# Performance work log

Measured on AMD Instinct MI355X. Metric: run time of the kernel, lower is better.

The kernel has to match this reference:

```python
import jax, jax.numpy as jnp
import numpy as np

WS = 8          # window size
HEADS = 2
EPS = 1e-5      # torch LayerNorm default

def setup_inputs() -> dict:
    key = jax.random.key(0)
    ks = jax.random.split(key, 8)
    B, C, H, W = 4, 64, 512, 512
    hid = 128
    s = 0.02
    return {
        "x": jax.random.normal(ks[0], (B, C, H, W), jnp.float32),
        "norm1_g": jnp.ones((C,), jnp.float32),
        "norm1_b": jnp.zeros((C,), jnp.float32),
        "in_w": s * jax.random.normal(ks[1], (3 * C, C), jnp.float32),
        "in_b": jnp.zeros((3 * C,), jnp.float32),
        "out_w": s * jax.random.normal(ks[2], (C, C), jnp.float32),
        "out_b": jnp.zeros((C,), jnp.float32),
        "proj_w": s * jax.random.normal(ks[3], (C, C), jnp.float32),
        "proj_b": jnp.zeros((C,), jnp.float32),
        "norm2_g": jnp.ones((C,), jnp.float32),
        "norm2_b": jnp.zeros((C,), jnp.float32),
        "mlp_w1": s * jax.random.normal(ks[4], (hid, C), jnp.float32),
        "mlp_b1": jnp.zeros((hid,), jnp.float32),
        "mlp_w2": s * jax.random.normal(ks[5], (C, hid), jnp.float32),
        "mlp_b2": jnp.zeros((C,), jnp.float32),
    }

def _ln(t, g, b):
    m = jnp.mean(t, axis=-1, keepdims=True)
    v = jnp.mean(jnp.square(t - m), axis=-1, keepdims=True)
    return (t - m) * jax.lax.rsqrt(v + EPS) * g + b

def _block(x, norm1_g, norm1_b, in_w, in_b, out_w, out_b,
           proj_w, proj_b, norm2_g, norm2_b, mlp_w1, mlp_b1, mlp_w2, mlp_b2):
    B, C, H, W = x.shape
    ws = WS
    # H, W divisible by ws => pad_h = pad_w = 0 (module pads otherwise)
    # window partition: (B,C,H,W) -> (B*nWh*nWw, ws*ws, C)
    t = x.reshape(B, C, H // ws, ws, W // ws, ws)
    t = jnp.transpose(t, (0, 2, 4, 3, 5, 1))            # (B, nWh, nWw, ws, ws, C)
    tokens = t.reshape(-1, ws * ws, C)                  # (nw, T, C)
    nw, T, _ = tokens.shape
    dh = C // HEADS

    tn = _ln(tokens, norm1_g, norm1_b)
    # packed qkv projection (torch MultiheadAttention in_proj)
    qkv = tn @ in_w.T + in_b                            # (nw, T, 3C)
    q, k, v = jnp.split(qkv, 3, axis=-1)
    q = q.reshape(nw, T, HEADS, dh)
    k = k.reshape(nw, T, HEADS, dh)
    v = v.reshape(nw, T, HEADS, dh)
    scale = 1.0 / jnp.sqrt(jnp.asarray(dh, x.dtype))
    scores = jnp.einsum('nqhd,nkhd->nhqk', q, k) * scale  # (nw, H, T, T)
    attn = jax.nn.softmax(scores, axis=-1)
    o = jnp.einsum('nhqk,nkhd->nqhd', attn, v).reshape(nw, T, C)
    o = o @ out_w.T + out_b                             # MHA out_proj
    o = o @ proj_w.T + proj_b                           # extra proj
    tokens = tokens + o

    tn2 = _ln(tokens, norm2_g, norm2_b)
    h = jax.nn.gelu(tn2 @ mlp_w1.T + mlp_b1, approximate=False)
    tokens = tokens + (h @ mlp_w2.T + mlp_b2)

    # window reverse: (nw, T, C) -> (B, C, H, W)
    t = tokens.reshape(B, H // ws, W // ws, ws, ws, C)
    t = jnp.transpose(t, (0, 5, 1, 3, 2, 4))
    return t.reshape(B, C, H, W)

def reference(x, norm1_g, norm1_b, in_w, in_b, out_w, out_b,
              proj_w, proj_b, norm2_g, norm2_b, mlp_w1, mlp_b1, mlp_w2, mlp_b2):
    return _block(x, norm1_g, norm1_b, in_w, in_b, out_w, out_b,
                  proj_w, proj_b, norm2_g, norm2_b, mlp_w1, mlp_b1, mlp_w2, mlp_b2)
```

## Files before the change

kernel.cpp:

```cpp
#include <hip/hip_runtime.h>
#include <math.h>

#define HWs (512*512)

typedef short  s8v __attribute__((ext_vector_type(8)));
typedef short  s4v __attribute__((ext_vector_type(4)));
typedef float  f4v __attribute__((ext_vector_type(4)));

__device__ __forceinline__ float lo16(unsigned int u){ union{unsigned int i; float f;} z; z.i=u<<16;         return z.f; }
__device__ __forceinline__ float hi16(unsigned int u){ union{unsigned int i; float f;} z; z.i=u&0xffff0000u; return z.f; }
__device__ __forceinline__ unsigned int cvtpk(float lo, float hi){
  unsigned int r; asm("v_cvt_pk_bf16_f32 %0, %1, %2" : "=v"(r) : "v"(lo), "v"(hi)); return r;
}
__device__ __forceinline__ unsigned short f2bf_rne(float f){
  union{float g; unsigned int u;} a; a.g=f;
  unsigned int r = a.u + 0x7fffu + ((a.u>>16)&1u);
  return (unsigned short)(r>>16);
}
__device__ __forceinline__ void st8(void* p, unsigned int a, unsigned int b){
  union{ unsigned int u[2]; s4v v; } z; z.u[0]=a; z.u[1]=b;
  *(s4v*)p = z.v;
}
__device__ __forceinline__ void st16(void* p, unsigned int a, unsigned int b, unsigned int c, unsigned int d){
  union{ unsigned int u[4]; s8v v; } z; z.u[0]=a; z.u[1]=b; z.u[2]=c; z.u[3]=d;
  *(s8v*)p = z.v;
}

#define SWZ(row) (((((row)&7) ^ (((row)>>3)&7)))<<4)

__global__ void conv_wb(const float* __restrict__ inw, const float* __restrict__ w1,
                        const float* __restrict__ w2, unsigned short* __restrict__ ws){
  int i = blockIdx.x*256 + threadIdx.x;
  if (i < 12288)      ws[i] = f2bf_rne(inw[i]);
  else if (i < 20480) ws[i] = f2bf_rne(w1[i-12288]);
  else                ws[i] = f2bf_rne(w2[i-20480]);
}

__global__ void fuse_proj_kernel(const float* __restrict__ out_w, const float* __restrict__ out_b,
                                 const float* __restrict__ proj_w, const float* __restrict__ proj_b,
                                 unsigned short* __restrict__ wf_bf, float* __restrict__ bfv){
  int i = blockIdx.x*256 + threadIdx.x;
  if (i >= 64*64) return;
  int c = i>>6, k = i&63;
  float acc = 0.f;
  for (int m=0;m<64;m++) acc += proj_w[c*64+m]*out_w[m*64+k];
  wf_bf[i] = f2bf_rne(acc);
  if (k==0){
    float ab = proj_b[c];
    for (int m=0;m<64;m++) ab += proj_w[c*64+m]*out_b[m];
    bfv[c] = ab;
  }
}

__global__ __launch_bounds__(512,4) void hat_main(
    const float* __restrict__ x,
    const float* __restrict__ n1g, const float* __restrict__ n1b,
    const float* __restrict__ inb,
    const unsigned short* __restrict__ wbf,
    const float* __restrict__ bfv,
    const float* __restrict__ n2g, const float* __restrict__ n2b,
    const float* __restrict__ b1, const float* __restrict__ b2,
    float* __restrict__ out)
{
  __shared__ __align__(16) unsigned char lds[65536];
  #define RA 0
  #define RB 8192
  #define RC 16384
  #define RD 24576

  const int t = threadIdx.x;
  const int l = t & 63;
  const int g = (l>>4)&3, c = l&15;
  const int w  = t>>6;
  const int tm = w>>1;
  const int wb = (w&1)<<15;
  const int cb = t>>7;
  const int pr = (t>>4)&7;
  const int pc = t&15;
  const int tok = pr*8 + (pc&7);
  const int wtb = ((pc>>3)&1)<<15;

  const int n = blockIdx.x;
  const int ww2 = n&31, wh=(n>>5)&63, b=n>>11;
  const size_t pix = (size_t)(wh*8+pr)*512 + ww2*16 + pc;
  const float* xp = x + ((size_t)b*64 + 16*cb)*HWs + pix;

  const unsigned short* inw_bf = wbf;
  const unsigned short* w1_bf  = wbf + 12288;
  const unsigned short* w2_bf  = wbf + 20480;
  const unsigned short* wf_bf  = wbf + 28672;

  float xr[16];
  #pragma unroll
  for (int i=0;i<16;i++) xr[i] = xp[(size_t)i*HWs];
  {
    float s1=0.f, s2=0.f;
    #pragma unroll
    for (int i=0;i<16;i++){ s1 += xr[i]; s2 += xr[i]*xr[i]; }
    *(float2*)(lds + wtb + RD + tok*32 + cb*8) = make_float2(s1, s2);
  }
  __syncthreads();

  unsigned int xres[8];
  {
    float S=0.f, SS=0.f;
    #pragma unroll
    for (int grp=0; grp<4; grp++){
      float2 p = *(const float2*)(lds + wtb + RD + tok*32 + grp*8);
      S += p.x; SS += p.y;
    }
    float mu = S*(1.f/64.f);
    float var = SS*(1.f/64.f) - mu*mu;
    float rstd = rsqrtf(var + 1e-5f);
    float tv[16];
    #pragma unroll
    for (int i=0;i<16;i++) tv[i] = (xr[i]-mu)*rstd*n1g[16*cb+i] + n1b[16*cb+i];
    #pragma unroll
    for (int j=0;j<8;j++) xres[j] = cvtpk(xr[2*j], xr[2*j+1]);
    int sw = SWZ(tok);
    st16(lds + wtb + RA + tok*128 + ((32*cb   ) ^ sw),
         cvtpk(tv[0],tv[1]), cvtpk(tv[2],tv[3]), cvtpk(tv[4],tv[5]), cvtpk(tv[6],tv[7]));
    st16(lds + wtb + RA + tok*128 + ((32*cb+16) ^ sw),
         cvtpk(tv[8],tv[9]), cvtpk(tv[10],tv[11]), cvtpk(tv[12],tv[13]), cvtpk(tv[14],tv[15]));
  }
  __syncthreads();

  const int row_a = 16*tm + c;
  const int swa = SWZ(row_a);
  const float scale = 0.17677669529663688f;

  s8v a0 = *(const s8v*)(lds + wb + RA + row_a*128 + ((16*g   ) ^ swa));
  s8v a1 = *(const s8v*)(lds + wb + RA + row_a*128 + ((64+16*g) ^ swa));
  #pragma unroll 1
  for (int chunk=0; chunk<2; chunk++){
    f4v acc[4] = {};
    #pragma unroll
    for (int tn=0;tn<4;tn++){
      s8v wf0 = *(const s8v*)(inw_bf + (64*chunk+16*tn+c)*64 + 8*g);
      s8v wf1 = *(const s8v*)(inw_bf + (64*chunk+16*tn+c)*64 + 32 + 8*g);
      acc[tn] = __builtin_amdgcn_mfma_f32_16x16x32_bf16(wf0, a0, acc[tn], 0,0,0);
      acc[tn] = __builtin_amdgcn_mfma_f32_16x16x32_bf16(wf1, a1, acc[tn], 0,0,0);
    }
    const int reg = (chunk==0) ? RB : RC;
    #pragma unroll
    for (int tn=0;tn<4;tn++){
      float4 b4 = *(const float4*)(inb + 64*chunk + 16*tn + 4*g);
      float v0=acc[tn][0]+b4.x, v1=acc[tn][1]+b4.y, v2=acc[tn][2]+b4.z, v3=acc[tn][3]+b4.w;
      if (chunk==0){ v0*=scale; v1*=scale; v2*=scale; v3*=scale; }
      st8(lds + wb + reg + row_a*128 + ((2*(16*tn+4*g)) ^ swa), cvtpk(v0,v1), cvtpk(v2,v3));
    }
  }
  {
    f4v acc[4] = {};
    #pragma unroll
    for (int tn=0;tn<4;tn++){
      s8v wf0 = *(const s8v*)(inw_bf + (128+16*tn+c)*64 + 8*g);
      s8v wf1 = *(const s8v*)(inw_bf + (128+16*tn+c)*64 + 32 + 8*g);
      acc[tn] = __builtin_amdgcn_mfma_f32_16x16x32_bf16(a0, wf0, acc[tn], 0,0,0);
      acc[tn] = __builtin_amdgcn_mfma_f32_16x16x32_bf16(a1, wf1, acc[tn], 0,0,0);
    }
    #pragma unroll
    for (int tn=0;tn<4;tn++){
      int drow = 16*tn + c;
      float bias = inb[128 + drow];
      st8(lds + wb + RD + drow*128 + ((2*(16*tm+4*g)) ^ SWZ(drow)),
          cvtpk(acc[tn][0]+bias, acc[tn][1]+bias), cvtpk(acc[tn][2]+bias, acc[tn][3]+bias));
    }
  }
  __syncthreads();

  #pragma unroll 1
  for (int h=0; h<2; h++){
    s8v qa = *(const s8v*)(lds + wb + RB + row_a*128 + ((64*h+16*g) ^ swa));
    f4v sacc[4] = {};
    #pragma unroll
    for (int tn=0;tn<4;tn++){
      int kr = 16*tn + c;
      s8v kb = *(const s8v*)(lds + wb + RC + kr*128 + ((64*h+16*g) ^ SWZ(kr)));
      sacc[tn] = __builtin_amdgcn_mfma_f32_16x16x32_bf16(kb, qa, sacc[tn], 0,0,0);
    }
    float mt[4];
    #pragma unroll
    for (int tn=0;tn<4;tn++)
      mt[tn] = fmaxf(fmaxf(sacc[tn][0],sacc[tn][1]), fmaxf(sacc[tn][2],sacc[tn][3]));
    float m = fmaxf(fmaxf(mt[0],mt[1]), fmaxf(mt[2],mt[3]));
    m = fmaxf(m, __shfl_xor(m, 16));
    m = fmaxf(m, __shfl_xor(m, 32));
    float lsum = 0.f;
    float p[4][4];
    #pragma unroll
    for (int tn=0;tn<4;tn++)
      #pragma unroll
      for (int r=0;r<4;r++){ float e = __expf(sacc[tn][r]-m); p[tn][r]=e; lsum+=e; }
    lsum += __shfl_xor(lsum, 16);
    lsum += __shfl_xor(lsum, 32);
    float inv = 1.f/lsum;
    #pragma unroll
    for (int tn=0;tn<4;tn++)
      st8(lds + wb + RA + row_a*128 + ((2*(16*tn+4*g)) ^ swa),
          cvtpk(p[tn][0]*inv, p[tn][1]*inv), cvtpk(p[tn][2]*inv, p[tn][3]*inv));
    asm volatile("" ::: "memory");
    s8v pa0 = *(const s8v*)(lds + wb + RA + row_a*128 + ((16*g   ) ^ swa));
    s8v pa1 = *(const s8v*)(lds + wb + RA + row_a*128 + ((64+16*g) ^ swa));
    #pragma unroll
    for (int tnl=0; tnl<2; tnl++){
      int vr = 32*h + 16*tnl + c;
      int svr = SWZ(vr);
      s8v vb0 = *(const s8v*)(lds + wb + RD + vr*128 + ((16*g   ) ^ svr));
      s8v vb1 = *(const s8v*)(lds + wb + RD + vr*128 + ((64+16*g) ^ svr));
      f4v oc = {};
      oc = __builtin_amdgcn_mfma_f32_16x16x32_bf16(vb0, pa0, oc, 0,0,0);
      oc = __builtin_amdgcn_mfma_f32_16x16x32_bf16(vb1, pa1, oc, 0,0,0);
      st8(lds + wb + RB + row_a*128 + ((64*h + 32*tnl + 8*g) ^ swa),
          cvtpk(oc[0], oc[1]), cvtpk(oc[2], oc[3]));
    }
  }
  __syncthreads();

  {
    s8v oa0 = *(const s8v*)(lds + wb + RB + row_a*128 + ((16*g   ) ^ swa));
    s8v oa1 = *(const s8v*)(lds + wb + RB + row_a*128 + ((64+16*g) ^ swa));
    f4v acc[4] = {};
    #pragma unroll
    for (int tn=0;tn<4;tn++){
      s8v wf0 = *(const s8v*)(wf_bf + (16*tn+c)*64 + 8*g);
      s8v wf1 = *(const s8v*)(wf_bf + (16*tn+c)*64 + 32 + 8*g);
      acc[tn] = __builtin_amdgcn_mfma_f32_16x16x32_bf16(wf0, oa0, acc[tn], 0,0,0);
      acc[tn] = __builtin_amdgcn_mfma_f32_16x16x32_bf16(wf1, oa1, acc[tn], 0,0,0);
    }
    #pragma unroll
    for (int tn=0;tn<4;tn++){
      float4 b4 = *(const float4*)(bfv + 16*tn + 4*g);
      st8(lds + wb + RC + row_a*128 + ((2*(16*tn+4*g)) ^ swa),
          cvtpk(acc[tn][0]+b4.x, acc[tn][1]+b4.y), cvtpk(acc[tn][2]+b4.z, acc[tn][3]+b4.w));
    }
  }
  __syncthreads();

  float row2[16];
  {
    int sw = SWZ(tok);
    uint4 A0 = *(const uint4*)(lds + wtb + RC + tok*128 + ((32*cb   ) ^ sw));
    uint4 A1 = *(const uint4*)(lds + wtb + RC + tok*128 + ((32*cb+16) ^ sw));
    unsigned int pr8[8] = {A0.x,A0.y,A0.z,A0.w,A1.x,A1.y,A1.z,A1.w};
    #pragma unroll
    for (int j=0;j<8;j++){
      row2[2*j]   = lo16(pr8[j]) + lo16(xres[j]);
      row2[2*j+1] = hi16(pr8[j]) + hi16(xres[j]);
    }
    float s1=0.f, s2=0.f;
    #pragma unroll
    for (int i=0;i<16;i++){ s1 += row2[i]; s2 += row2[i]*row2[i]; }
    *(float2*)(lds + wtb + RB + tok*32 + cb*8) = make_float2(s1, s2);
  }
  __syncthreads();
  {
    float S=0.f, SS=0.f;
    #pragma unroll
    for (int grp=0; grp<4; grp++){
      float2 p = *(const float2*)(lds + wtb + RB + tok*32 + grp*8);
      S += p.x; SS += p.y;
    }
    float mu2 = S*(1.f/64.f);
    float v2 = SS*(1.f/64.f) - mu2*mu2;
    float rstd2 = rsqrtf(v2 + 1e-5f);
    float tv[16];
    #pragma unroll
    for (int i=0;i<16;i++) tv[i] = (row2[i]-mu2)*rstd2*n2g[16*cb+i] + n2b[16*cb+i];
    int sw = SWZ(tok);
    st16(lds + wtb + RA + tok*128 + ((32*cb   ) ^ sw),
         cvtpk(tv[0],tv[1]), cvtpk(tv[2],tv[3]), cvtpk(tv[4],tv[5]), cvtpk(tv[6],tv[7]));
    st16(lds + wtb + RA + tok*128 + ((32*cb+16) ^ sw),
         cvtpk(tv[8],tv[9]), cvtpk(tv[10],tv[11]), cvtpk(tv[12],tv[13]), cvtpk(tv[14],tv[15]));
  }
  __syncthreads();

  {
    s8v la0 = *(const s8v*)(lds + wb + RA + row_a*128 + ((16*g   ) ^ swa));
    s8v la1 = *(const s8v*)(lds + wb + RA + row_a*128 + ((64+16*g) ^ swa));
    #pragma unroll 1
    for (int nch=0; nch<2; nch++){
      f4v acc[4] = {};
      #pragma unroll
      for (int tn=0;tn<4;tn++){
        s8v wf0 = *(const s8v*)(w1_bf + (64*nch+16*tn+c)*64 + 8*g);
        s8v wf1 = *(const s8v*)(w1_bf + (64*nch+16*tn+c)*64 + 32 + 8*g);
        acc[tn] = __builtin_amdgcn_mfma_f32_16x16x32_bf16(wf0, la0, acc[tn], 0,0,0);
        acc[tn] = __builtin_amdgcn_mfma_f32_16x16x32_bf16(wf1, la1, acc[tn], 0,0,0);
      }
      const int reg = nch ? RD : RB;
      #pragma unroll
      for (int tn=0;tn<4;tn++){
        float4 b4 = *(const float4*)(b1 + 64*nch + 16*tn + 4*g);
        float vv[4] = {acc[tn][0]+b4.x, acc[tn][1]+b4.y, acc[tn][2]+b4.z, acc[tn][3]+b4.w};
        #pragma unroll
        for (int r=0;r<4;r++){
          float v = vv[r];
          float z = v*(1.595769122f + 0.071354816f*v*v);
          vv[r] = v/(1.f + __expf(-z));
        }
        st8(lds + wb + reg + row_a*128 + ((2*(16*tn+4*g)) ^ swa), cvtpk(vv[0],vv[1]), cvtpk(vv[2],vv[3]));
      }
    }
  }
  asm volatile("" ::: "memory");
  {
    f4v acc[4] = {};
    #pragma unroll
    for (int kk=0;kk<4;kk++){
      const int reg = (kk<2) ? RB : RD;
      s8v ha = *(const s8v*)(lds + wb + reg + row_a*128 + ((64*(kk&1)+16*g) ^ swa));
      #pragma unroll
      for (int tn=0;tn<4;tn++){
        s8v wf = *(const s8v*)(w2_bf + (16*tn+c)*128 + 32*kk + 8*g);
        acc[tn] = __builtin_amdgcn_mfma_f32_16x16x32_bf16(wf, ha, acc[tn], 0,0,0);
      }
    }
    #pragma unroll
    for (int tn=0;tn<4;tn++){
      float4 b4 = *(const float4*)(b2 + 16*tn + 4*g);
      st8(lds + wb + RA + row_a*128 + ((2*(16*tn+4*g)) ^ swa),
          cvtpk(acc[tn][0]+b4.x, acc[tn][1]+b4.y), cvtpk(acc[tn][2]+b4.z, acc[tn][3]+b4.w));
    }
  }
  __syncthreads();

  {
    int sw = SWZ(tok);
    uint4 A0 = *(const uint4*)(lds + wtb + RA + tok*128 + ((32*cb   ) ^ sw));
    uint4 A1 = *(const uint4*)(lds + wtb + RA + tok*128 + ((32*cb+16) ^ sw));
    unsigned int pr8[8] = {A0.x,A0.y,A0.z,A0.w,A1.x,A1.y,A1.z,A1.w};
    float* op = out + ((size_t)b*64 + 16*cb)*HWs + pix;
    #pragma unroll
    for (int j=0;j<8;j++){
      op[(size_t)(2*j  )*HWs] = lo16(pr8[j]) + row2[2*j];
      op[(size_t)(2*j+1)*HWs] = hi16(pr8[j]) + row2[2*j+1];
    }
  }
}

extern "C" void kernel_launch(void* const* d_in, const int* in_sizes, int n_in,
                              void* d_out, int out_size, void* d_ws, size_t ws_size,
                              hipStream_t stream) {
  const float* x    = (const float*)d_in[0];
  const float* n1g  = (const float*)d_in[1];
  const float* n1b  = (const float*)d_in[2];
  const float* inw  = (const float*)d_in[3];
  const float* inb  = (const float*)d_in[4];
  const float* outw = (const float*)d_in[5];
  const float* outb = (const float*)d_in[6];
  const float* pw   = (const float*)d_in[7];
  const float* pb   = (const float*)d_in[8];
  const float* n2g  = (const float*)d_in[9];
  const float* n2b  = (const float*)d_in[10];
  const float* w1   = (const float*)d_in[11];
  const float* b1   = (const float*)d_in[12];
  const float* w2   = (const float*)d_in[13];
  const float* b2   = (const float*)d_in[14];

  unsigned short* wsu = (unsigned short*)d_ws;
  unsigned short* wf_bf = wsu + 28672;
  float* bfv = (float*)((char*)d_ws + 65536);

  hipLaunchKernelGGL(conv_wb, dim3(112), dim3(256), 0, stream, inw, w1, w2, wsu);
  hipLaunchKernelGGL(fuse_proj_kernel, dim3(16), dim3(256), 0, stream, outw, outb, pw, pb, wf_bf, bfv);
  hipLaunchKernelGGL(hat_main, dim3(8192), dim3(512), 0, stream,
                     x, n1g, n1b, inb, wsu, bfv, n2g, n2b, b1, b2, (float*)d_out);
}
```

Measured before the change: 648.8 us.

## Process one window per 256-thread block and reduce LayerNorm stats via shuffles

Each block previously handled two 8x8 windows with 512 threads and 64KB of LDS. Now each block handles a single window with 256 threads and 32KB LDS, launching twice as many blocks. The thread mapping is changed so that the four channel-group threads for a token sit in the same wavefront. This lets both LayerNorm statistic reductions use shuffles and removes two LDS round-trips and barriers. Global loads now cover 8 contiguous pixels per row instead of 16, which may reduce coalescing width.

Result: slower. 735.0 us (+13.3%).

```diff
diff --git a/kernel.cpp b/kernel.cpp
--- a/kernel.cpp
+++ b/kernel.cpp
@@ -52,7 +52,7 @@
   }
 }
 
-__global__ __launch_bounds__(512,4) void hat_main(
+__global__ __launch_bounds__(256,5) void hat_main(
     const float* __restrict__ x,
     const float* __restrict__ n1g, const float* __restrict__ n1b,
     const float* __restrict__ inb,
@@ -62,7 +62,7 @@
     const float* __restrict__ b1, const float* __restrict__ b2,
     float* __restrict__ out)
 {
-  __shared__ __align__(16) unsigned char lds[65536];
+  __shared__ __align__(16) unsigned char lds[32768];
   #define RA 0
   #define RB 8192
   #define RC 16384
@@ -71,18 +71,15 @@
   const int t = threadIdx.x;
   const int l = t & 63;
   const int g = (l>>4)&3, c = l&15;
-  const int w  = t>>6;
-  const int tm = w>>1;
-  const int wb = (w&1)<<15;
-  const int cb = t>>7;
-  const int pr = (t>>4)&7;
-  const int pc = t&15;
-  const int tok = pr*8 + (pc&7);
-  const int wtb = ((pc>>3)&1)<<15;
+  const int tm = t>>6;
+  const int s  = t&7;
+  const int cb = (t>>3)&3;
+  const int r  = ((t>>6)<<1) | ((t>>5)&1);
+  const int tok = r*8 + s;
 
   const int n = blockIdx.x;
-  const int ww2 = n&31, wh=(n>>5)&63, b=n>>11;
-  const size_t pix = (size_t)(wh*8+pr)*512 + ww2*16 + pc;
+  const int ww = n&63, wh=(n>>6)&63, b=n>>12;
+  const size_t pix = (size_t)(wh*8+r)*512 + ww*8 + s;
   const float* xp = x + ((size_t)b*64 + 16*cb)*HWs + pix;
 
   const unsigned short* inw_bf = wbf;
@@ -93,24 +90,15 @@
   float xr[16];
   #pragma unroll
   for (int i=0;i<16;i++) xr[i] = xp[(size_t)i*HWs];
+  unsigned int xres[8];
   {
     float s1=0.f, s2=0.f;
     #pragma unroll
     for (int i=0;i<16;i++){ s1 += xr[i]; s2 += xr[i]*xr[i]; }
-    *(float2*)(lds + wtb + RD + tok*32 + cb*8) = make_float2(s1, s2);
-  }
-  __syncthreads();
-
-  unsigned int xres[8];
-  {
-    float S=0.f, SS=0.f;
-    #pragma unroll
-    for (int grp=0; grp<4; grp++){
-      float2 p = *(const float2*)(lds + wtb + RD + tok*32 + grp*8);
-      S += p.x; SS += p.y;
-    }
-    float mu = S*(1.f/64.f);
-    float var = SS*(1.f/64.f) - mu*mu;
+    s1 += __shfl_xor(s1, 8);  s2 += __shfl_xor(s2, 8);
+    s1 += __shfl_xor(s1, 16); s2 += __shfl_xor(s2, 16);
+    float mu = s1*(1.f/64.f);
+    float var = s2*(1.f/64.f) - mu*mu;
     float rstd = rsqrtf(var + 1e-5f);
     float tv[16];
     #pragma unroll
@@ -118,9 +106,9 @@
     #pragma unroll
     for (int j=0;j<8;j++) xres[j] = cvtpk(xr[2*j], xr[2*j+1]);
     int sw = SWZ(tok);
-    st16(lds + wtb + RA + tok*128 + ((32*cb   ) ^ sw),
+    st16(lds + RA + tok*128 + ((32*cb   ) ^ sw),
          cvtpk(tv[0],tv[1]), cvtpk(tv[2],tv[3]), cvtpk(tv[4],tv[5]), cvtpk(tv[6],tv[7]));
-    st16(lds + wtb + RA + tok*128 + ((32*cb+16) ^ sw),
+    st16(lds + RA + tok*128 + ((32*cb+16) ^ sw),
          cvtpk(tv[8],tv[9]), cvtpk(tv[10],tv[11]), cvtpk(tv[12],tv[13]), cvtpk(tv[14],tv[15]));
   }
   __syncthreads();
@@ -129,8 +117,8 @@
   const int swa = SWZ(row_a);
   const float scale = 0.17677669529663688f;
 
-  s8v a0 = *(const s8v*)(lds + wb + RA + row_a*128 + ((16*g   ) ^ swa));
-  s8v a1 = *(const s8v*)(lds + wb + RA + row_a*128 + ((64+16*g) ^ swa));
+  s8v a0 = *(const s8v*)(lds + RA + row_a*128 + ((16*g   ) ^ swa));
+  s8v a1 = *(const s8v*)(lds + RA + row_a*128 + ((64+16*g) ^ swa));
   #pragma unroll 1
   for (int chunk=0; chunk<2; chunk++){
     f4v acc[4] = {};
@@ -147,7 +135,7 @@
       float4 b4 = *(const float4*)(inb + 64*chunk + 16*tn + 4*g);
       float v0=acc[tn][0]+b4.x, v1=acc[tn][1]+b4.y, v2=acc[tn][2]+b4.z, v3=acc[tn][3]+b4.w;
       if (chunk==0){ v0*=scale; v1*=scale; v2*=scale; v3*=scale; }
-      st8(lds + wb + reg + row_a*128 + ((2*(16*tn+4*g)) ^ swa), cvtpk(v0,v1), cvtpk(v2,v3));
+      st8(lds + reg + row_a*128 + ((2*(16*tn+4*g)) ^ swa), cvtpk(v0,v1), cvtpk(v2,v3));
     }
   }
   {
@@ -163,7 +151,7 @@
     for (int tn=0;tn<4;tn++){
       int drow = 16*tn + c;
       float bias = inb[128 + drow];
-      st8(lds + wb + RD + drow*128 + ((2*(16*tm+4*g)) ^ SWZ(drow)),
+      st8(lds + RD + drow*128 + ((2*(16*tm+4*g)) ^ SWZ(drow)),
           cvtpk(acc[tn][0]+bias, acc[tn][1]+bias), cvtpk(acc[tn][2]+bias, acc[tn][3]+bias));
     }
   }
@@ -171,12 +159,12 @@
 
   #pragma unroll 1
   for (int h=0; h<2; h++){
-    s8v qa = *(const s8v*)(lds + wb + RB + row_a*128 + ((64*h+16*g) ^ swa));
+    s8v qa = *(const s8v*)(lds + RB + row_a*128 + ((64*h+16*g) ^ swa));
     f4v sacc[4] = {};
     #pragma unroll
     for (int tn=0;tn<4;tn++){
       int kr = 16*tn + c;
-      s8v kb = *(const s8v*)(lds + wb + RC + kr*128 + ((64*h+16*g) ^ SWZ(kr)));
+      s8v kb = *(const s8v*)(lds + RC + kr*128 + ((64*h+16*g) ^ SWZ(kr)));
       sacc[tn] = __builtin_amdgcn_mfma_f32_16x16x32_bf16(kb, qa, sacc[tn], 0,0,0);
     }
     float mt[4];
@@ -191,35 +179,35 @@
     #pragma unroll
     for (int tn=0;tn<4;tn++)
       #pragma unroll
-      for (int r=0;r<4;r++){ float e = __expf(sacc[tn][r]-m); p[tn][r]=e; lsum+=e; }
+      for (int rr=0;rr<4;rr++){ float e = __expf(sacc[tn][rr]-m); p[tn][rr]=e; lsum+=e; }
     lsum += __shfl_xor(lsum, 16);
     lsum += __shfl_xor(lsum, 32);
     float inv = 1.f/lsum;
     #pragma unroll
     for (int tn=0;tn<4;tn++)
-      st8(lds + wb + RA + row_a*128 + ((2*(16*tn+4*g)) ^ swa),
+      st8(lds + RA + row_a*128 + ((2*(16*tn+4*g)) ^ swa),
           cvtpk(p[tn][0]*inv, p[tn][1]*inv), cvtpk(p[tn][2]*inv, p[tn][3]*inv));
     asm volatile("" ::: "memory");
-    s8v pa0 = *(const s8v*)(lds + wb + RA + row_a*128 + ((16*g   ) ^ swa));
-    s8v pa1 = *(const s8v*)(lds + wb + RA + row_a*128 + ((64+16*g) ^ swa));
+    s8v pa0 = *(const s8v*)(lds + RA + row_a*128 + ((16*g   ) ^ swa));
+    s8v pa1 = *(const s8v*)(lds + RA + row_a*128 + ((64+16*g) ^ swa));
     #pragma unroll
     for (int tnl=0; tnl<2; tnl++){
       int vr = 32*h + 16*tnl + c;
       int svr = SWZ(vr);
-      s8v vb0 = *(const s8v*)(lds + wb + RD + vr*128 + ((16*g   ) ^ svr));
-      s8v vb1 = *(const s8v*)(lds + wb + RD + vr*128 + ((64+16*g) ^ svr));
+      s8v vb0 = *(const s8v*)(lds + RD + vr*128 + ((16*g   ) ^ svr));
+      s8v vb1 = *(const s8v*)(lds + RD + vr*128 + ((64+16*g) ^ svr));
       f4v oc = {};
       oc = __builtin_amdgcn_mfma_f32_16x16x32_bf16(vb0, pa0, oc, 0,0,0);
       oc = __builtin_amdgcn_mfma_f32_16x16x32_bf16(vb1, pa1, oc, 0,0,0);
-      st8(lds + wb + RB + row_a*128 + ((64*h + 32*tnl + 8*g) ^ swa),
+      st8(lds + RB + row_a*128 + ((64*h + 32*tnl + 8*g) ^ swa),
           cvtpk(oc[0], oc[1]), cvtpk(oc[2], oc[3]));
     }
   }
   __syncthreads();
 
   {
-    s8v oa0 = *(const s8v*)(lds + wb + RB + row_a*128 + ((16*g   ) ^ swa));
-    s8v oa1 = *(const s8v*)(lds + wb + RB + row_a*128 + ((64+16*g) ^ swa));
+    s8v oa0 = *(const s8v*)(lds + RB + row_a*128 + ((16*g   ) ^ swa));
+    s8v oa1 = *(const s8v*)(lds + RB + row_a*128 + ((64+16*g) ^ swa));
     f4v acc[4] = {};
     #pragma unroll
     for (int tn=0;tn<4;tn++){
@@ -231,7 +219,7 @@
     #pragma unroll
     for (int tn=0;tn<4;tn++){
       float4 b4 = *(const float4*)(bfv + 16*tn + 4*g);
-      st8(lds + wb + RC + row_a*128 + ((2*(16*tn+4*g)) ^ swa),
+      st8(lds + RC + row_a*128 + ((2*(16*tn+4*g)) ^ swa),
           cvtpk(acc[tn][0]+b4.x, acc[tn][1]+b4.y), cvtpk(acc[tn][2]+b4.z, acc[tn][3]+b4.w));
     }
   }
@@ -240,8 +228,8 @@
   float row2[16];
   {
     int sw = SWZ(tok);
-    uint4 A0 = *(const uint4*)(lds + wtb + RC + tok*128 + ((32*cb   ) ^ sw));
-    uint4 A1 = *(const uint4*)(lds + wtb + RC + tok*128 + ((32*cb+16) ^ sw));
+    uint4 A0 = *(const uint4*)(lds + RC + tok*128 + ((32*cb   ) ^ sw));
+    uint4 A1 = *(const uint4*)(lds + RC + tok*128 + ((32*cb+16) ^ sw));
     unsigned int pr8[8] = {A0.x,A0.y,A0.z,A0.w,A1.x,A1.y,A1.z,A1.w};
     #pragma unroll
     for (int j=0;j<8;j++){
@@ -251,33 +239,24 @@
     float s1=0.f, s2=0.f;
     #pragma unroll
     for (int i=0;i<16;i++){ s1 += row2[i]; s2 += row2[i]*row2[i]; }
-    *(float2*)(lds + wtb + RB + tok*32 + cb*8) = make_float2(s1, s2);
-  }
-  __syncthreads();
-  {
-    float S=0.f, SS=0.f;
-    #pragma unroll
-    for (int grp=0; grp<4; grp++){
-      float2 p = *(const float2*)(lds + wtb + RB + tok*32 + grp*8);
-      S += p.x; SS += p.y;
-    }
-    float mu2 = S*(1.f/64.f);
-    float v2 = SS*(1.f/64.f) - mu2*mu2;
+    s1 += __shfl_xor(s1, 8);  s2 += __shfl_xor(s2, 8);
+    s1 += __shfl_xor(s1, 16); s2 += __shfl_xor(s2, 16);
+    float mu2 = s1*(1.f/64.f);
+    float v2 = s2*(1.f/64.f) - mu2*mu2;
     float rstd2 = rsqrtf(v2 + 1e-5f);
     float tv[16];
     #pragma unroll
     for (int i=0;i<16;i++) tv[i] = (row2[i]-mu2)*rstd2*n2g[16*cb+i] + n2b[16*cb+i];
-    int sw = SWZ(tok);
-    st16(lds + wtb + RA + tok*128 + ((32*cb   ) ^ sw),
+    st16(lds + RA + tok*128 + ((32*cb   ) ^ sw),
          cvtpk(tv[0],tv[1]), cvtpk(tv[2],tv[3]), cvtpk(tv[4],tv[5]), cvtpk(tv[6],tv[7]));
-    st16(lds + wtb + RA + tok*128 + ((32*cb+16) ^ sw),
+    st16(lds + RA + tok*128 + ((32*cb+16) ^ sw),
          cvtpk(tv[8],tv[9]), cvtpk(tv[10],tv[11]), cvtpk(tv[12],tv[13]), cvtpk(tv[14],tv[15]));
   }
   __syncthreads();
 
   {
-    s8v la0 = *(const s8v*)(lds + wb + RA + row_a*128 + ((16*g   ) ^ swa));
-    s8v la1 = *(const s8v*)(lds + wb + RA + row_a*128 + ((64+16*g) ^ swa));
+    s8v la0 = *(const s8v*)(lds + RA + row_a*128 + ((16*g   ) ^ swa));
+    s8v la1 = *(const s8v*)(lds + RA + row_a*128 + ((64+16*g) ^ swa));
     #pragma unroll 1
     for (int nch=0; nch<2; nch++){
       f4v acc[4] = {};
@@ -294,12 +273,12 @@
         float4 b4 = *(const float4*)(b1 + 64*nch + 16*tn + 4*g);
         float vv[4] = {acc[tn][0]+b4.x, acc[tn][1]+b4.y, acc[tn][2]+b4.z, acc[tn][3]+b4.w};
         #pragma unroll
-        for (int r=0;r<4;r++){
-          float v = vv[r];
+        for (int rr=0;rr<4;rr++){
+          float v = vv[rr];
           float z = v*(1.595769122f + 0.071354816f*v*v);
-          vv[r] = v/(1.f + __expf(-z));
+          vv[rr] = v/(1.f + __expf(-z));
         }
-        st8(lds + wb + reg + row_a*128 + ((2*(16*tn+4*g)) ^ swa), cvtpk(vv[0],vv[1]), cvtpk(vv[2],vv[3]));
+        st8(lds + reg + row_a*128 + ((2*(16*tn+4*g)) ^ swa), cvtpk(vv[0],vv[1]), cvtpk(vv[2],vv[3]));
       }
     }
   }
@@ -309,7 +288,7 @@
     #pragma unroll
     for (int kk=0;kk<4;kk++){
       const int reg = (kk<2) ? RB : RD;
-      s8v ha = *(const s8v*)(lds + wb + reg + row_a*128 + ((64*(kk&1)+16*g) ^ swa));
+      s8v ha = *(const s8v*)(lds + reg + row_a*128 + ((64*(kk&1)+16*g) ^ swa));
       #pragma unroll
       for (int tn=0;tn<4;tn++){
         s8v wf = *(const s8v*)(w2_bf + (16*tn+c)*128 + 32*kk + 8*g);
@@ -319,7 +298,7 @@
     #pragma unroll
     for (int tn=0;tn<4;tn++){
       float4 b4 = *(const float4*)(b2 + 16*tn + 4*g);
-      st8(lds + wb + RA + row_a*128 + ((2*(16*tn+4*g)) ^ swa),
+      st8(lds + RA + row_a*128 + ((2*(16*tn+4*g)) ^ swa),
           cvtpk(acc[tn][0]+b4.x, acc[tn][1]+b4.y), cvtpk(acc[tn][2]+b4.z, acc[tn][3]+b4.w));
     }
   }
@@ -327,8 +306,8 @@
 
   {
     int sw = SWZ(tok);
-    uint4 A0 = *(const uint4*)(lds + wtb + RA + tok*128 + ((32*cb   ) ^ sw));
-    uint4 A1 = *(const uint4*)(lds + wtb + RA + tok*128 + ((32*cb+16) ^ sw));
+    uint4 A0 = *(const uint4*)(lds + RA + tok*128 + ((32*cb   ) ^ sw));
+    uint4 A1 = *(const uint4*)(lds + RA + tok*128 + ((32*cb+16) ^ sw));
     unsigned int pr8[8] = {A0.x,A0.y,A0.z,A0.w,A1.x,A1.y,A1.z,A1.w};
     float* op = out + ((size_t)b*64 + 16*cb)*HWs + pix;
     #pragma unroll
@@ -364,6 +343,6 @@
 
   hipLaunchKernelGGL(conv_wb, dim3(112), dim3(256), 0, stream, inw, w1, w2, wsu);
   hipLaunchKernelGGL(fuse_proj_kernel, dim3(16), dim3(256), 0, stream, outw, outb, pw, pb, wf_bf, bfv);
-  hipLaunchKernelGGL(hat_main, dim3(8192), dim3(512), 0, stream,
+  hipLaunchKernelGGL(hat_main, dim3(16384), dim3(256), 0, stream,
                      x, n1g, n1b, inb, wsu, bfv, n2g, n2b, b1, b2, (float*)d_out);
 }
```
